# Kernel tuning notes

Hardware: AMD Instinct MI355X
Metric: run time of the kernel (lower is better)

The kernel has to match this reference:

```python
import jax, jax.numpy as jnp
import numpy as np

NUM_EXPERTS = 16
TOPK = 2
NUM_SHARED = 2


def setup_inputs() -> dict:
    key = jax.random.key(0)
    k1, k2, k3, k4 = jax.random.split(key, 4)
    B, S, D = 4, 2048, 1024
    feat = jax.random.normal(k1, (B, S, D), dtype=jnp.float32)
    router_w = jax.random.normal(k2, (NUM_EXPERTS, D), dtype=jnp.float32) * 0.02
    shared_w = jax.random.normal(k3, (NUM_SHARED * D, D), dtype=jnp.float32) * 0.02
    expert_w = jax.random.normal(k4, (NUM_EXPERTS, D, D), dtype=jnp.float32) * 0.02
    return {"feat": feat, "router_w": router_w, "shared_w": shared_w, "expert_w": expert_w}


def reference(feat, router_w, shared_w, expert_w):
    B, S, D = feat.shape
    T = B * S
    x = feat.reshape(T, D)

    # router logits [T, E]
    logits = x @ router_w.T

    # shared experts: Linear(D, ns*D) then sum over the ns chunks
    shared = (x @ shared_w.T).reshape(T, NUM_SHARED, D).sum(axis=1)

    # gate_topk with norm_probs=True: top-k logits then softmax over them
    topk_vals, topk_idx = jax.lax.top_k(logits, TOPK)       # [T, k]
    weights = jax.nn.softmax(topk_vals, axis=-1)            # [T, k]

    # balance loss (training, token-level): fi = counts/(B*S), pi = mean softmax
    scores = jax.nn.softmax(logits, axis=-1)                # [T, E]
    counts = jnp.zeros((NUM_EXPERTS,), jnp.float32).at[topk_idx.reshape(-1)].add(1.0)
    fi = counts / T
    pi = scores.mean(axis=0)
    aux_loss = jnp.sum(pi * fi)

    # dense combine-weight matrix gate[t,e] = sum_k weights[t,k] * 1[idx[t,k]==e]
    gate = jnp.zeros((T, NUM_EXPERTS), jnp.float32).at[
        jnp.arange(T)[:, None], topk_idx
    ].add(weights)

    # all-expert compute then weighted combine (dense-MoE reference)
    # expert_out[t,e,h] = sum_d x[t,d] * expert_w[e,h,d]
    expert_out = jnp.einsum('td,ehd->teh', x, expert_w)
    moe = jnp.einsum('te,teh->th', gate, expert_out)

    out = (shared + moe).reshape(B, S, D)
    return out, aux_loss
```

## Files before the change

### kernel.cpp

```cpp
#include <hip/hip_runtime.h>
#include <stdint.h>

#define T_TOK 8192
#define DDIM  1024
#define NEXP  16
#define MAXTILES 144

typedef unsigned short u16;
typedef __attribute__((ext_vector_type(8))) short v8s;
typedef __attribute__((ext_vector_type(4))) float v4f;

__device__ __forceinline__ u16 f2bf(float f) {
  union { float f; unsigned u; } v; v.f = f;
  unsigned r = v.u + 0x7fffu + ((v.u >> 16) & 1u);
  return (u16)(r >> 16);
}

__device__ __forceinline__ void gload_lds16(const u16* gsrc, u16* ldst) {
  typedef __attribute__((address_space(1))) const void GV;
  typedef __attribute__((address_space(3))) void LV;
  __builtin_amdgcn_global_load_lds((GV*)(uintptr_t)gsrc, (LV*)(uintptr_t)ldst, 16, 0, 0);
}

__global__ __launch_bounds__(256) void k_cvt4(const float4* __restrict__ in,
                                              ushort4* __restrict__ out, int n4) {
  int i = blockIdx.x * 256 + threadIdx.x;
  if (i >= n4) return;
  float4 v = in[i];
  ushort4 o; o.x = f2bf(v.x); o.y = f2bf(v.y); o.z = f2bf(v.z); o.w = f2bf(v.w);
  out[i] = o;
}

__global__ __launch_bounds__(256) void k_cvt_shared(const float4* __restrict__ sw,
                                                    ushort4* __restrict__ out, int n4) {
  int i = blockIdx.x * 256 + threadIdx.x;
  if (i >= n4) return;
  float4 a = sw[i];
  float4 b = sw[i + n4];
  ushort4 o;
  o.x = f2bf(a.x + b.x); o.y = f2bf(a.y + b.y);
  o.z = f2bf(a.z + b.z); o.w = f2bf(a.w + b.w);
  out[i] = o;
}

__global__ __launch_bounds__(256) void k_router(const float* __restrict__ x,
                                                const float* __restrict__ rw,
                                                int* __restrict__ topkI,
                                                float* __restrict__ topkW,
                                                int* __restrict__ counts,
                                                float* __restrict__ piSum) {
  __shared__ float lds_pi[NEXP];
  __shared__ int   lds_cnt[NEXP];
  int tid = threadIdx.x;
  if (tid < NEXP) { lds_pi[tid] = 0.f; lds_cnt[tid] = 0; }
  __syncthreads();
  int lane = tid & 63, wave = tid >> 6;

  for (int ti = 0; ti < 8; ++ti) {
    int t = blockIdx.x * 32 + wave * 8 + ti;
    const float* xr = x + (size_t)t * DDIM;
    float xv[16];
#pragma unroll
    for (int i = 0; i < 16; ++i) xv[i] = xr[i * 64 + lane];
    float lg[NEXP];
#pragma unroll
    for (int e = 0; e < NEXP; ++e) {
      const float* wr = rw + (size_t)e * DDIM;
      float p = 0.f;
#pragma unroll
      for (int i = 0; i < 16; ++i) p += xv[i] * wr[i * 64 + lane];
#pragma unroll
      for (int off = 32; off > 0; off >>= 1) p += __shfl_xor(p, off);
      lg[e] = p;
    }
    float mx = lg[0];
#pragma unroll
    for (int e = 1; e < NEXP; ++e) mx = fmaxf(mx, lg[e]);
    float sum = 0.f;
#pragma unroll
    for (int e = 0; e < NEXP; ++e) sum += __expf(lg[e] - mx);
    float v0 = lg[0]; int i0 = 0;
#pragma unroll
    for (int e = 1; e < NEXP; ++e) if (lg[e] > v0) { v0 = lg[e]; i0 = e; }
    float v1 = -3.0e38f; int i1 = 0;
#pragma unroll
    for (int e = 0; e < NEXP; ++e) if (e != i0 && lg[e] > v1) { v1 = lg[e]; i1 = e; }
    float e1 = __expf(v1 - v0);
    float w0 = 1.f / (1.f + e1);
    float w1 = e1 / (1.f + e1);
    if (lane == 0) {
      topkI[2 * t] = i0; topkI[2 * t + 1] = i1;
      topkW[2 * t] = w0; topkW[2 * t + 1] = w1;
      atomicAdd(&lds_cnt[i0], 1); atomicAdd(&lds_cnt[i1], 1);
    }
#pragma unroll
    for (int e = 0; e < NEXP; ++e)
      if (lane == e) atomicAdd(&lds_pi[e], __expf(lg[e] - mx) / sum);
  }
  __syncthreads();
  if (tid < NEXP) {
    atomicAdd(&counts[tid], lds_cnt[tid]);
    atomicAdd(&piSum[tid], lds_pi[tid]);
  }
}

__global__ void k_finalize(const int* __restrict__ counts, const float* __restrict__ piSum,
                           int* __restrict__ offs, int* __restrict__ meta,
                           int* __restrict__ ntile, int* __restrict__ cursor,
                           float* __restrict__ outAux) {
  if (threadIdx.x != 0) return;
  int off = 0;
  for (int e = 0; e < NEXP; ++e) { offs[e] = off; off += counts[e]; }
  offs[NEXP] = off;
  int nt = 0;
  for (int e = 0; e < NEXP; ++e) {
    for (int rs = 0; rs < counts[e]; rs += 128) { meta[2 * nt] = e; meta[2 * nt + 1] = rs; ++nt; }
    cursor[e] = 0;
  }
  ntile[0] = nt;
  float aux = 0.f;
  for (int e = 0; e < NEXP; ++e)
    aux += (piSum[e] / (float)T_TOK) * ((float)counts[e] / (float)T_TOK);
  outAux[0] = aux;
}

__global__ __launch_bounds__(256) void k_scatter(const int* __restrict__ topkI,
                                                 const float* __restrict__ topkW,
                                                 const int* __restrict__ offs,
                                                 int* __restrict__ cursor,
                                                 int* __restrict__ rowTok,
                                                 float* __restrict__ rowW) {
  __shared__ int lcnt[NEXP], lbase[NEXP];
  int tid = threadIdx.x;
  if (tid < NEXP) lcnt[tid] = 0;
  __syncthreads();
  int p = blockIdx.x * 256 + tid;
  int e = topkI[p];
  int myLocal = atomicAdd(&lcnt[e], 1);
  __syncthreads();
  if (tid < NEXP) lbase[tid] = atomicAdd(&cursor[tid], lcnt[tid]);
  __syncthreads();
  int dst = offs[e] + lbase[e] + myLocal;
  rowTok[dst] = p >> 1;
  rowW[dst] = topkW[p];
}

__global__ __launch_bounds__(256) void k_gemm(const u16* __restrict__ xb,
                                              const u16* __restrict__ wb,
                                              const int* __restrict__ meta,
                                              const int* __restrict__ ntile,
                                              const int* __restrict__ offs,
                                              const int* __restrict__ rowTok,
                                              const float* __restrict__ rowW,
                                              float* __restrict__ out, int mode) {
  __shared__ u16 As[128 * 32];
  __shared__ u16 Bs[128 * 32];
  int tid = threadIdx.x;
  int lane = tid & 63, wave = tid >> 6;
  int tileN = blockIdx.y;

  int e, rowStart, offBase = 0, cnt = 128;
  if (mode == 0) {
    e = NEXP; rowStart = blockIdx.x * 128;
  } else {
    int ti = blockIdx.x;
    if (ti >= ntile[0]) return;
    e = meta[2 * ti]; rowStart = meta[2 * ti + 1];
    offBase = offs[e]; cnt = offs[e + 1] - offBase;
  }

  int sRow = tid >> 2;
  int sChunk = tid & 3;
  int tok0, tok1;
  if (mode == 0) {
    tok0 = rowStart + sRow; tok1 = rowStart + 64 + sRow;
  } else {
    int r0 = min(rowStart + sRow, cnt - 1);
    int r1 = min(rowStart + 64 + sRow, cnt - 1);
    tok0 = rowTok[offBase + r0]; tok1 = rowTok[offBase + r1];
  }
  const u16* wbase = wb + (size_t)e * (DDIM * DDIM) + (size_t)(tileN * 128) * DDIM;
  const u16* aSrc0 = xb + (size_t)tok0 * DDIM + sChunk * 8;
  const u16* aSrc1 = xb + (size_t)tok1 * DDIM + sChunk * 8;
  const u16* bSrc0 = wbase + (size_t)sRow * DDIM + sChunk * 8;
  const u16* bSrc1 = wbase + (size_t)(64 + sRow) * DDIM + sChunk * 8;
  u16* aDst0 = As + wave * 512;
  u16* aDst1 = As + 2048 + wave * 512;
  u16* bDst0 = Bs + wave * 512;
  u16* bDst1 = Bs + 2048 + wave * 512;

  v4f acc[4][4];
#pragma unroll
  for (int m = 0; m < 4; ++m)
#pragma unroll
    for (int n = 0; n < 4; ++n) acc[m][n] = (v4f)0.f;

  int wm = (wave >> 1) * 64, wn = (wave & 1) * 64;
  int rsel = lane & 15;
  int kb = (lane >> 4) * 8;

  for (int kk = 0; kk < DDIM / 32; ++kk) {
    int k0 = kk * 32;
    __syncthreads();
    gload_lds16(aSrc0 + k0, aDst0);
    gload_lds16(aSrc1 + k0, aDst1);
    gload_lds16(bSrc0 + k0, bDst0);
    gload_lds16(bSrc1 + k0, bDst1);
    __syncthreads();

    v8s af[4], bfr[4];
#pragma unroll
    for (int m = 0; m < 4; ++m)
      af[m] = *(const v8s*)(As + (wm + m * 16 + rsel) * 32 + kb);
#pragma unroll
    for (int n = 0; n < 4; ++n)
      bfr[n] = *(const v8s*)(Bs + (wn + n * 16 + rsel) * 32 + kb);
#pragma unroll
    for (int m = 0; m < 4; ++m)
#pragma unroll
      for (int n = 0; n < 4; ++n)
        acc[m][n] = __builtin_amdgcn_mfma_f32_16x16x32_bf16(af[m], bfr[n], acc[m][n], 0, 0, 0);
  }

  int colBase = tileN * 128 + wn + (lane & 15);
  if (mode == 0) {
#pragma unroll
    for (int m = 0; m < 4; ++m) {
      int rBase = rowStart + wm + m * 16 + (lane >> 4) * 4;
#pragma unroll
      for (int n = 0; n < 4; ++n) {
        v4f a = acc[m][n];
        int col = colBase + n * 16;
#pragma unroll
        for (int j = 0; j < 4; ++j)
          out[(size_t)(rBase + j) * DDIM + col] = a[j];
      }
    }
  } else {
#pragma unroll
    for (int m = 0; m < 4; ++m) {
      int rloc = rowStart + wm + m * 16 + (lane >> 4) * 4;
#pragma unroll
      for (int j = 0; j < 4; ++j) {
        int r = rloc + j;
        if (r < cnt) {
          int idx = offBase + r;
          int t = rowTok[idx];
          float w = rowW[idx];
          float* orow = out + (size_t)t * DDIM;
#pragma unroll
          for (int n = 0; n < 4; ++n)
            atomicAdd(orow + colBase + n * 16, w * acc[m][n][j]);
        }
      }
    }
  }
}

extern "C" void kernel_launch(void* const* d_in, const int* in_sizes, int n_in,
                              void* d_out, int out_size, void* d_ws, size_t ws_size,
                              hipStream_t stream) {
  const float* feat = (const float*)d_in[0];
  const float* rw   = (const float*)d_in[1];
  const float* sw   = (const float*)d_in[2];
  const float* ew   = (const float*)d_in[3];
  float* out = (float*)d_out;
  char* ws = (char*)d_ws;

  u16* xb = (u16*)(ws + 0);
  u16* wb = (u16*)(ws + 16777216);
  char* smallBase = ws + 52428800;
  int*   counts = (int*)(smallBase + 0);
  float* piSum  = (float*)(smallBase + 64);
  int*   cursor = (int*)(smallBase + 128);
  int*   ntile  = (int*)(smallBase + 192);
  int*   topkI  = (int*)(ws + 52429056);
  float* topkW  = (float*)(ws + 52494592);
  int*   offs   = (int*)(ws + 52560128);
  int*   rowTok = (int*)(ws + 52560256);
  float* rowW   = (float*)(ws + 52625792);
  int*   meta   = (int*)(ws + 52691328);

  hipMemsetAsync(smallBase, 0, 256, stream);

  k_cvt4<<<8192, 256, 0, stream>>>((const float4*)feat, (ushort4*)xb, 2097152);
  k_cvt4<<<16384, 256, 0, stream>>>((const float4*)ew, (ushort4*)wb, 4194304);
  k_cvt_shared<<<1024, 256, 0, stream>>>((const float4*)sw,
                                         (ushort4*)(wb + (size_t)NEXP * DDIM * DDIM), 262144);

  k_router<<<256, 256, 0, stream>>>(feat, rw, topkI, topkW, counts, piSum);
  k_finalize<<<1, 64, 0, stream>>>(counts, piSum, offs, meta, ntile, cursor, out + 8388608);
  k_scatter<<<64, 256, 0, stream>>>(topkI, topkW, offs, cursor, rowTok, rowW);

  dim3 gShared(64, 8), gExpert(MAXTILES, 8);
  k_gemm<<<gShared, 256, 0, stream>>>(xb, wb, meta, ntile, offs, rowTok, rowW, out, 0);
  k_gemm<<<gExpert, 256, 0, stream>>>(xb, wb, meta, ntile, offs, rowTok, rowW, out, 1);
}
```

Before: 369.8 us.

## Fuse shared and expert GEMMs into one launch with double-buffered LDS

Shared-expert tiles are now listed in the tile metadata next to the routed-expert tiles, so one GEMM launch covers both. The K loop uses two LDS buffers: the next slice is prefetched with global_load_lds while the current one feeds the MFMAs, leaving one barrier per iteration. The LDS layout is reorganised into k-chunk-major order, and launch bounds now request 4 waves per SIMD. In exchange, the shared-expert output is written with atomics into an output that must first be zeroed by a full memset, which adds memory traffic.

```diff
diff --git a/kernel.cpp b/kernel.cpp
--- a/kernel.cpp
+++ b/kernel.cpp
@@ -4,7 +4,7 @@
 #define T_TOK 8192
 #define DDIM  1024
 #define NEXP  16
-#define MAXTILES 144
+#define MAXT  208
 
 typedef unsigned short u16;
 typedef __attribute__((ext_vector_type(8))) short v8s;
@@ -113,6 +113,7 @@
   for (int e = 0; e < NEXP; ++e) { offs[e] = off; off += counts[e]; }
   offs[NEXP] = off;
   int nt = 0;
+  for (int rs = 0; rs < T_TOK; rs += 128) { meta[2 * nt] = NEXP; meta[2 * nt + 1] = rs; ++nt; }
   for (int e = 0; e < NEXP; ++e) {
     for (int rs = 0; rs < counts[e]; rs += 128) { meta[2 * nt] = e; meta[2 * nt + 1] = rs; ++nt; }
     cursor[e] = 0;
@@ -145,49 +146,35 @@
   rowW[dst] = topkW[p];
 }
 
-__global__ __launch_bounds__(256) void k_gemm(const u16* __restrict__ xb,
-                                              const u16* __restrict__ wb,
-                                              const int* __restrict__ meta,
-                                              const int* __restrict__ ntile,
-                                              const int* __restrict__ offs,
-                                              const int* __restrict__ rowTok,
-                                              const float* __restrict__ rowW,
-                                              float* __restrict__ out, int mode) {
-  __shared__ u16 As[128 * 32];
-  __shared__ u16 Bs[128 * 32];
+__global__ __launch_bounds__(256, 4) void k_gemm(const u16* __restrict__ xb,
+                                                 const u16* __restrict__ wb,
+                                                 const int* __restrict__ meta,
+                                                 const int* __restrict__ ntile,
+                                                 const int* __restrict__ offs,
+                                                 const int* __restrict__ rowTok,
+                                                 const float* __restrict__ rowW,
+                                                 float* __restrict__ out) {
+  __shared__ u16 As[2][4096];
+  __shared__ u16 Bs[2][4096];
   int tid = threadIdx.x;
+  int ti = blockIdx.x;
+  if (ti >= ntile[0]) return;
   int lane = tid & 63, wave = tid >> 6;
   int tileN = blockIdx.y;
 
-  int e, rowStart, offBase = 0, cnt = 128;
-  if (mode == 0) {
-    e = NEXP; rowStart = blockIdx.x * 128;
+  int e = meta[2 * ti], rowStart = meta[2 * ti + 1];
+  int offBase = 0, cnt;
+  int srow = tid & 127;
+  int kc8 = (tid >> 7) * 8;
+  int tok;
+  if (e == NEXP) {
+    cnt = T_TOK; tok = rowStart + srow;
   } else {
-    int ti = blockIdx.x;
-    if (ti >= ntile[0]) return;
-    e = meta[2 * ti]; rowStart = meta[2 * ti + 1];
     offBase = offs[e]; cnt = offs[e + 1] - offBase;
-  }
-
-  int sRow = tid >> 2;
-  int sChunk = tid & 3;
-  int tok0, tok1;
-  if (mode == 0) {
-    tok0 = rowStart + sRow; tok1 = rowStart + 64 + sRow;
-  } else {
-    int r0 = min(rowStart + sRow, cnt - 1);
-    int r1 = min(rowStart + 64 + sRow, cnt - 1);
-    tok0 = rowTok[offBase + r0]; tok1 = rowTok[offBase + r1];
-  }
-  const u16* wbase = wb + (size_t)e * (DDIM * DDIM) + (size_t)(tileN * 128) * DDIM;
-  const u16* aSrc0 = xb + (size_t)tok0 * DDIM + sChunk * 8;
-  const u16* aSrc1 = xb + (size_t)tok1 * DDIM + sChunk * 8;
-  const u16* bSrc0 = wbase + (size_t)sRow * DDIM + sChunk * 8;
-  const u16* bSrc1 = wbase + (size_t)(64 + sRow) * DDIM + sChunk * 8;
-  u16* aDst0 = As + wave * 512;
-  u16* aDst1 = As + 2048 + wave * 512;
-  u16* bDst0 = Bs + wave * 512;
-  u16* bDst1 = Bs + 2048 + wave * 512;
+    tok = rowTok[offBase + min(rowStart + srow, cnt - 1)];
+  }
+  const u16* aRow = xb + (size_t)tok * DDIM + kc8;
+  const u16* bRow = wb + (size_t)e * (DDIM * DDIM) + (size_t)(tileN * 128 + srow) * DDIM + kc8;
 
   v4f acc[4][4];
 #pragma unroll
@@ -197,61 +184,56 @@
 
   int wm = (wave >> 1) * 64, wn = (wave & 1) * 64;
   int rsel = lane & 15;
-  int kb = (lane >> 4) * 8;
-
-  for (int kk = 0; kk < DDIM / 32; ++kk) {
-    int k0 = kk * 32;
-    __syncthreads();
-    gload_lds16(aSrc0 + k0, aDst0);
-    gload_lds16(aSrc1 + k0, aDst1);
-    gload_lds16(bSrc0 + k0, bDst0);
-    gload_lds16(bSrc1 + k0, bDst1);
-    __syncthreads();
+  int q = lane >> 4;
+
+#define STAGE(buf, k0)                                              \
+  do {                                                              \
+    gload_lds16(aRow + (k0),      &As[buf][wave * 512]);            \
+    gload_lds16(aRow + (k0) + 16, &As[buf][2048 + wave * 512]);     \
+    gload_lds16(bRow + (k0),      &Bs[buf][wave * 512]);            \
+    gload_lds16(bRow + (k0) + 16, &Bs[buf][2048 + wave * 512]);     \
+  } while (0)
+
+  STAGE(0, 0);
+  __syncthreads();
+
+  int cur = 0;
+  for (int t = 0; t < DDIM / 32; ++t) {
+    if (t + 1 < DDIM / 32) STAGE(cur ^ 1, (t + 1) * 32);
 
     v8s af[4], bfr[4];
 #pragma unroll
     for (int m = 0; m < 4; ++m)
-      af[m] = *(const v8s*)(As + (wm + m * 16 + rsel) * 32 + kb);
+      af[m] = *(const v8s*)&As[cur][(q * 128 + wm + m * 16 + rsel) * 8];
 #pragma unroll
     for (int n = 0; n < 4; ++n)
-      bfr[n] = *(const v8s*)(Bs + (wn + n * 16 + rsel) * 32 + kb);
+      bfr[n] = *(const v8s*)&Bs[cur][(q * 128 + wn + n * 16 + rsel) * 8];
 #pragma unroll
     for (int m = 0; m < 4; ++m)
 #pragma unroll
       for (int n = 0; n < 4; ++n)
         acc[m][n] = __builtin_amdgcn_mfma_f32_16x16x32_bf16(af[m], bfr[n], acc[m][n], 0, 0, 0);
-  }
-
-  int colBase = tileN * 128 + wn + (lane & 15);
-  if (mode == 0) {
-#pragma unroll
-    for (int m = 0; m < 4; ++m) {
-      int rBase = rowStart + wm + m * 16 + (lane >> 4) * 4;
-#pragma unroll
-      for (int n = 0; n < 4; ++n) {
-        v4f a = acc[m][n];
-        int col = colBase + n * 16;
-#pragma unroll
-        for (int j = 0; j < 4; ++j)
-          out[(size_t)(rBase + j) * DDIM + col] = a[j];
-      }
-    }
-  } else {
-#pragma unroll
-    for (int m = 0; m < 4; ++m) {
-      int rloc = rowStart + wm + m * 16 + (lane >> 4) * 4;
-#pragma unroll
-      for (int j = 0; j < 4; ++j) {
-        int r = rloc + j;
-        if (r < cnt) {
-          int idx = offBase + r;
-          int t = rowTok[idx];
-          float w = rowW[idx];
-          float* orow = out + (size_t)t * DDIM;
-#pragma unroll
-          for (int n = 0; n < 4; ++n)
-            atomicAdd(orow + colBase + n * 16, w * acc[m][n][j]);
-        }
+
+    __syncthreads();
+    cur ^= 1;
+  }
+#undef STAGE
+
+  int colBase = tileN * 128 + wn + rsel;
+#pragma unroll
+  for (int m = 0; m < 4; ++m) {
+    int rloc = rowStart + wm + m * 16 + q * 4;
+#pragma unroll
+    for (int j = 0; j < 4; ++j) {
+      int r = rloc + j;
+      if (r < cnt) {
+        int t; float w;
+        if (e == NEXP) { t = r; w = 1.f; }
+        else { t = rowTok[offBase + r]; w = rowW[offBase + r]; }
+        float* orow = out + (size_t)t * DDIM;
+#pragma unroll
+        for (int n = 0; n < 4; ++n)
+          atomicAdd(orow + colBase + n * 16, w * acc[m][n][j]);
       }
     }
   }
@@ -282,6 +264,7 @@
   int*   meta   = (int*)(ws + 52691328);
 
   hipMemsetAsync(smallBase, 0, 256, stream);
+  hipMemsetAsync(out, 0, (size_t)out_size * sizeof(float), stream);
 
   k_cvt4<<<8192, 256, 0, stream>>>((const float4*)feat, (ushort4*)xb, 2097152);
   k_cvt4<<<16384, 256, 0, stream>>>((const float4*)ew, (ushort4*)wb, 4194304);
@@ -292,7 +275,6 @@
   k_finalize<<<1, 64, 0, stream>>>(counts, piSum, offs, meta, ntile, cursor, out + 8388608);
   k_scatter<<<64, 256, 0, stream>>>(topkI, topkW, offs, cursor, rowTok, rowW);
 
-  dim3 gShared(64, 8), gExpert(MAXTILES, 8);
-  k_gemm<<<gShared, 256, 0, stream>>>(xb, wb, meta, ntile, offs, rowTok, rowW, out, 0);
-  k_gemm<<<gExpert, 256, 0, stream>>>(xb, wb, meta, ntile, offs, rowTok, rowW, out, 1);
-}
+  dim3 gFused(MAXT, 8);
+  k_gemm<<<gFused, 256, 0, stream>>>(xb, wb, meta, ntile, offs, rowTok, rowW, out);
+}
```

New measurement: 403.8 us. +9.2%, slower.
